# Kernel optimization log

Hardware: AMD Instinct MI355X
Metric: run time of the kernel (lower is better)

## Reference

```python
import jax, jax.numpy as jnp
import numpy as np

NEG_INF = -9e15  # matches torch's -9000000000000000.0 mask value
ALPHA = 0.2      # LeakyReLU negative slope


def setup_inputs() -> dict:
    key = jax.random.key(0)
    k1, k2, k3, k4 = jax.random.split(key, 4)
    B, N, Fin, Fout = 8, 2048, 256, 256
    h = jax.random.normal(k1, (B, N, Fin), dtype=jnp.float32)
    adj = jax.random.randint(k2, (B, N, N), 0, 2, dtype=jnp.int32)
    # xavier_uniform with gain=1.414
    limW = 1.414 * np.sqrt(6.0 / (Fin + Fout))
    W = jax.random.uniform(k3, (Fin, Fout), minval=-limW, maxval=limW, dtype=jnp.float32)
    lima = 1.414 * np.sqrt(6.0 / (2 * Fout + 1))
    a = jax.random.uniform(k4, (2 * Fout, 1), minval=-lima, maxval=lima, dtype=jnp.float32)
    return {"h": h, "adj": adj, "W": W, "a": a}


def reference(h, adj, W, a):
    # h: (B, N, Fin), adj: (B, N, N), W: (Fin, Fout), a: (2*Fout, 1)
    Fout = W.shape[1]
    Wh = jnp.einsum('bni,io->bno', h, W)                 # (B, N, Fout)
    # e[b,i,j] = leakyrelu(Wh[b,i] @ a1 + Wh[b,j] @ a2) -- equivalent to the
    # original concat([Wh_i, Wh_j]) @ a without the O(N^2 * 2F) intermediate.
    e1 = Wh @ a[:Fout, 0]                                # (B, N)
    e2 = Wh @ a[Fout:, 0]                                # (B, N)
    e = jax.nn.leaky_relu(e1[:, :, None] + e2[:, None, :], negative_slope=ALPHA)
    masked = jnp.where(adj > 0, e, NEG_INF)
    attention = jax.nn.softmax(masked, axis=-1)          # (B, N, N)
    # dropout omitted (deterministic eval-mode reference)
    h_prime = jnp.einsum('bij,bjo->bio', attention, Wh)  # (B, N, Fout)
    return jax.nn.elu(h_prime), attention
```

## Files before the change

kernel.cpp:

```cpp
#include <hip/hip_runtime.h>
#include <hip/hip_bf16.h>
#include <stdint.h>

#define NEG_INF -9.0e15f
#define LRELU_ALPHA 0.2f
#define LOG2E 1.442695040888963f

using bf16x8  = __attribute__((ext_vector_type(8))) short;
using f32x4   = __attribute__((ext_vector_type(4))) float;
using short4v = __attribute__((ext_vector_type(4))) short;
using int4v   = __attribute__((ext_vector_type(4))) int;
using float4v = __attribute__((ext_vector_type(4))) float;
using uint2v  = __attribute__((ext_vector_type(2))) unsigned;
using uint4v  = __attribute__((ext_vector_type(4))) unsigned;

static __device__ __forceinline__ short f2bf(float f) {
  unsigned u = __builtin_bit_cast(unsigned, f);
  u = u + 0x7FFFu + ((u >> 16) & 1u);
  return (short)(u >> 16);
}
static __device__ __forceinline__ unsigned cvtpk_bf16(float lo, float hi) {
  unsigned r;
  asm volatile("v_cvt_pk_bf16_f32 %0, %1, %2" : "=v"(r) : "v"(lo), "v"(hi));
  return r;
}
static __device__ __forceinline__ void gload16(const void* g, void* l) {
  __builtin_amdgcn_global_load_lds((const __attribute__((address_space(1))) void*)g,
                                   (__attribute__((address_space(3))) void*)l, 16, 0, 0);
}

__global__ __launch_bounds__(256) void prep_kernel(
    const float* __restrict__ W, const float* __restrict__ a,
    short* __restrict__ W_t, float* __restrict__ aW1, float* __restrict__ aW2)
{
  const int bid = blockIdx.x;
  const int tid = threadIdx.x;
  if (bid < 16) {
    __shared__ float t[64][65];
    const int m0 = (bid & 3) * 64, n0 = (bid >> 2) * 64;
    const int rr = tid >> 3, cc = (tid & 7) * 8;
#pragma unroll
    for (int p = 0; p < 2; ++p) {
      int row = rr + p * 32;
      const float* sp = W + (m0 + row) * 256 + n0 + cc;
      float4v v0 = *(const float4v*)sp;
      float4v v1 = *(const float4v*)(sp + 4);
#pragma unroll
      for (int j = 0; j < 4; ++j) { t[row][cc + j] = v0[j]; t[row][cc + 4 + j] = v1[j]; }
    }
    __syncthreads();
#pragma unroll
    for (int p = 0; p < 2; ++p) {
      int orow = rr + p * 32;
      short vv[8] __attribute__((aligned(16)));
#pragma unroll
      for (int j = 0; j < 8; ++j) vv[j] = f2bf(t[cc + j][orow]);
      short* dp = W_t + (n0 + orow) * 256 + m0 + cc;
      *(int4v*)dp = *(const int4v*)vv;
    }
  } else {
    const int r8 = tid >> 3, o4 = (tid & 7) * 4;
    float s1[8] = {}, s2[8] = {};
#pragma unroll
    for (int rp = 0; rp < 8; ++rp) {
      int row = r8 + rp * 32;
#pragma unroll
      for (int k = 0; k < 8; ++k) {
        int o = o4 + k * 32;
        float4v wv = *(const float4v*)(W + row * 256 + o);
        float4v a1 = *(const float4v*)(a + o);
        float4v a2 = *(const float4v*)(a + 256 + o);
#pragma unroll
        for (int e = 0; e < 4; ++e) { s1[rp] += wv[e] * a1[e]; s2[rp] += wv[e] * a2[e]; }
      }
    }
#pragma unroll
    for (int rp = 0; rp < 8; ++rp) {
#pragma unroll
      for (int off = 4; off > 0; off >>= 1) {
        s1[rp] += __shfl_xor(s1[rp], off, 64);
        s2[rp] += __shfl_xor(s2[rp], off, 64);
      }
      if ((tid & 7) == 0) { aW1[r8 + rp * 32] = s1[rp]; aW2[r8 + rp * 32] = s2[rp]; }
    }
  }
}

__global__ __launch_bounds__(256) void evec2_kernel(
    const float* __restrict__ h, const float* __restrict__ aW1,
    const float* __restrict__ aW2, float* __restrict__ e1, float* __restrict__ e2)
{
  const int wid = threadIdx.x >> 6, lane = threadIdx.x & 63;
  const long long r = (long long)blockIdx.x * 4 + wid;
  float4v hv  = *(const float4v*)(h + r * 256 + lane * 4);
  float4v a1v = *(const float4v*)(aW1 + lane * 4);
  float4v a2v = *(const float4v*)(aW2 + lane * 4);
  float s1 = 0.f, s2 = 0.f;
#pragma unroll
  for (int k = 0; k < 4; ++k) { s1 += hv[k] * a1v[k]; s2 += hv[k] * a2v[k]; }
#pragma unroll
  for (int off = 32; off > 0; off >>= 1) {
    s1 += __shfl_xor(s1, off, 64);
    s2 += __shfl_xor(s2, off, 64);
  }
  if (lane == 0) { e1[r] = s1; e2[r] = s2; }
}

__global__ __launch_bounds__(256) void gemm_h_kernel(
    const float* __restrict__ A, const short* __restrict__ Bt,
    short* __restrict__ Wht)
{
  __shared__ short As[128 * 32];
  __shared__ short Bs[128 * 32];
  __shared__ short T[128][136];
  const int m0 = blockIdx.x * 128, n0 = blockIdx.y * 128;
  const int tid = threadIdx.x;
  const int w = tid >> 6, lane = tid & 63;
  const int wr = w >> 1, wc = w & 1;
  const int g = lane >> 4, lr = lane & 15;

  f32x4 acc[4][4] = {};

  for (int k0 = 0; k0 < 256; k0 += 32) {
    __syncthreads();
#pragma unroll
    for (int q = 0; q < 2; ++q) {
      int c = q * 256 + tid;
      int row = c >> 2, kq = (c & 3) << 3;
      const float* ap = A + (long long)(m0 + row) * 256 + k0 + kq;
      float4v u0 = *(const float4v*)ap;
      float4v u1 = *(const float4v*)(ap + 4);
      uint4v uv;
      uv[0] = cvtpk_bf16(u0[0], u0[1]);
      uv[1] = cvtpk_bf16(u0[2], u0[3]);
      uv[2] = cvtpk_bf16(u1[0], u1[1]);
      uv[3] = cvtpk_bf16(u1[2], u1[3]);
      *(bf16x8*)(As + c * 8) = __builtin_bit_cast(bf16x8, uv);
    }
#pragma unroll
    for (int q = 0; q < 2; ++q) {
      int p = w * 2 + q;
      int c = p * 64 + lane;
      int row = c >> 2, kq = (c & 3) << 3;
      gload16(Bt + (long long)(n0 + row) * 256 + k0 + kq, Bs + p * 512);
    }
    __syncthreads();

    bf16x8 af[4], bfr[4];
#pragma unroll
    for (int i = 0; i < 4; ++i) {
      af[i]  = *(const bf16x8*)(As + (wr * 64 + i * 16 + lr) * 32 + 8 * g);
      bfr[i] = *(const bf16x8*)(Bs + (wc * 64 + i * 16 + lr) * 32 + 8 * g);
    }
#pragma unroll
    for (int i = 0; i < 4; ++i)
#pragma unroll
      for (int j = 0; j < 4; ++j)
        acc[i][j] = __builtin_amdgcn_mfma_f32_16x16x32_bf16(af[i], bfr[j], acc[i][j], 0, 0, 0);
  }

  __syncthreads();
#pragma unroll
  for (int i = 0; i < 4; ++i) {
    int row_base = wr * 64 + i * 16 + 4 * g;
#pragma unroll
    for (int j = 0; j < 4; ++j) {
      int col = wc * 64 + j * 16 + lr;
#pragma unroll
      for (int r = 0; r < 4; ++r)
        T[col][row_base + r] = f2bf(acc[i][j][r]);
    }
  }
  __syncthreads();
  const int b = m0 >> 11, mloc = m0 & 2047;
  short* wb = Wht + (long long)b * 524288 + mloc;
#pragma unroll
  for (int p = 0; p < 8; ++p) {
    int c = (tid >> 4) + p * 16;
    int off = (tid & 15) * 8;
    bf16x8 v = *(const bf16x8*)(&T[c][off]);
    *(bf16x8*)(wb + (long long)(n0 + c) * 2048 + off) = v;
  }
}

__global__ __launch_bounds__(256) void pack_stats_kernel(
    const int* __restrict__ adj, const float* __restrict__ e1,
    const float* __restrict__ e2, unsigned char* __restrict__ mask,
    float* __restrict__ Lr, float* __restrict__ Dr)
{
  const int i = blockIdx.x;
  const int b = blockIdx.y;
  const long long row = (long long)b * 2048 + i;
  const int tid = threadIdx.x;
  const int wid = tid >> 6, lane = tid & 63;
  const int j0 = tid * 8;

  const int*   arow = adj + row * 2048 + j0;
  const float  ei   = e1[row];
  const float* e2b  = e2 + b * 2048 + j0;

  int4v   a0 = *(const int4v*)(arow);
  int4v   a1 = *(const int4v*)(arow + 4);
  float4v f0 = *(const float4v*)(e2b);
  float4v f1 = *(const float4v*)(e2b + 4);

  float s[8]; unsigned byte = 0u;
#pragma unroll
  for (int k = 0; k < 8; ++k) {
    float x = ei + (k < 4 ? f0[k] : f1[k - 4]);
    float v = fmaxf(x, LRELU_ALPHA * x);
    int  ad = (k < 4 ? a0[k] : a1[k - 4]);
    if (ad > 0) { s[k] = v; byte |= (1u << k); } else s[k] = NEG_INF;
  }
  float m = s[0];
#pragma unroll
  for (int k = 1; k < 8; ++k) m = fmaxf(m, s[k]);
#pragma unroll
  for (int off = 32; off > 0; off >>= 1) m = fmaxf(m, __shfl_xor(m, off, 64));

  __shared__ float wmax[4], wsum[4];
  if (lane == 0) wmax[wid] = m;
  __syncthreads();
  const float M = fmaxf(fmaxf(wmax[0], wmax[1]), fmaxf(wmax[2], wmax[3]));
  const bool empty = (M == NEG_INF);

  mask[row * 256 + tid] = empty ? (unsigned char)0xFF : (unsigned char)byte;

  float t = 0.f;
#pragma unroll
  for (int k = 0; k < 8; ++k) t += __expf(s[k] - M);
#pragma unroll
  for (int off = 32; off > 0; off >>= 1) t += __shfl_xor(t, off, 64);
  if (lane == 0) wsum[wid] = t;
  __syncthreads();
  if (tid == 0) {
    const float S = wsum[0] + wsum[1] + wsum[2] + wsum[3];
    Lr[row] = empty ? 0.0f : LOG2E;
    Dr[row] = empty ? -11.0f : (-M * LOG2E - __log2f(S));
  }
}

__global__ __launch_bounds__(256, 4) void pv_kernel(
    const unsigned char* __restrict__ mask, const float* __restrict__ e1,
    const float* __restrict__ e2, const float* __restrict__ Lr,
    const float* __restrict__ Dr, const short* __restrict__ Bt,
    float* __restrict__ attnw, float* __restrict__ C)
{
  __shared__ short As0[32 * 32],  As1[32 * 32];
  __shared__ short Bs0[256 * 32], Bs1[256 * 32];
  const int bid = blockIdx.x;
  const int bz  = bid & 7;
  const int M0  = (bid >> 3) << 5;
  const int tid = threadIdx.x;
  const int w = tid >> 6, lane = tid & 63;
  const int g = lane >> 4, lr = lane & 15;

  const long long rb = (long long)bz * 2048;
  Bt    += (long long)bz * 524288;
  attnw += (long long)bz * 4194304;
  C     += (long long)bz * 524288;

  const int pr = tid >> 3, k4 = (tid & 7) << 2;
  const int prow = M0 + pr;
  const float E1p = e1[rb + prow];
  const float Lp  = Lr[rb + prow];
  const float Dp  = Dr[rb + prow];
  const unsigned char* mrow = mask + (rb + prow) * 256;
  float* arow = attnw + (long long)prow * 2048;
  const int kc = k4 >> 3;
  const int as_off = pr * 32 + ((kc ^ ((pr >> 1) & 3)) << 3) + (k4 & 7);
  const float* e2b = e2 + rb;

  const int bcol_off = lane >> 2;
  const int bchunk   = (lane & 3) ^ ((lane >> 3) & 3);

  f32x4 acc[2][4] = {};

  auto STAGE = [&](short* BsD, short* AsD, int k0) {
#pragma unroll
    for (int q = 0; q < 4; ++q) {
      int pp = w * 4 + q;
      int col = pp * 16 + bcol_off;
      gload16(Bt + (long long)col * 2048 + k0 + bchunk * 8, BsD + pp * 512);
    }
    const unsigned by = (unsigned)(mrow[(k0 + k4) >> 3] >> (k4 & 7)) & 0xFu;
    const int kk = k0 + k4;
    float4v ev = *(const float4v*)(e2b + kk);
    float p4[4];
#pragma unroll
    for (int e = 0; e < 4; ++e) {
      float x = E1p + ev[e];
      float v = fmaxf(x, LRELU_ALPHA * x);
      float P = __builtin_amdgcn_exp2f(fmaf(v, Lp, Dp));
      p4[e] = ((by >> e) & 1u) ? P : 0.0f;
    }
    float4v o;
#pragma unroll
    for (int e = 0; e < 4; ++e) o[e] = p4[e];
    *(float4v*)(arow + kk) = o;
    uint2v uv;
    uv[0] = cvtpk_bf16(p4[0], p4[1]);
    uv[1] = cvtpk_bf16(p4[2], p4[3]);
    *(uint2v*)(AsD + as_off) = uv;
  };

  auto COMPUTE = [&](const short* BsD, const short* AsD) {
    bf16x8 af[2], bfr[4];
#pragma unroll
    for (int i = 0; i < 2; ++i) {
      int row = i * 16 + lr;
      af[i] = *(const bf16x8*)(AsD + row * 32 + ((g ^ ((row >> 1) & 3)) << 3));
    }
#pragma unroll
    for (int j = 0; j < 4; ++j) {
      int col = w * 64 + j * 16 + lr;
      bfr[j] = *(const bf16x8*)(BsD + col * 32 + ((g ^ ((col >> 1) & 3)) << 3));
    }
#pragma unroll
    for (int i = 0; i < 2; ++i)
#pragma unroll
      for (int j = 0; j < 4; ++j)
        acc[i][j] = __builtin_amdgcn_mfma_f32_16x16x32_bf16(af[i], bfr[j], acc[i][j], 0, 0, 0);
  };

  STAGE(Bs0, As0, 0);
  __syncthreads();
  for (int t = 0; t < 64; t += 2) {
    STAGE(Bs1, As1, (t + 1) * 32);
    COMPUTE(Bs0, As0);
    __syncthreads();
    if (t + 2 < 64) STAGE(Bs0, As0, (t + 2) * 32);
    COMPUTE(Bs1, As1);
    __syncthreads();
  }

#pragma unroll
  for (int i = 0; i < 2; ++i) {
    int row_base = M0 + i * 16 + 4 * g;
#pragma unroll
    for (int j = 0; j < 4; ++j) {
      int col = w * 64 + j * 16 + lr;
#pragma unroll
      for (int r = 0; r < 4; ++r) {
        float v = acc[i][j][r];
        v = (v > 0.f) ? v : (__expf(v) - 1.f);
        C[(long long)(row_base + r) * 256 + col] = v;
      }
    }
  }
}

extern "C" void kernel_launch(void* const* d_in, const int* in_sizes, int n_in,
                              void* d_out, int out_size, void* d_ws, size_t ws_size,
                              hipStream_t stream)
{
  const float* h   = (const float*)d_in[0];
  const int*   adj = (const int*)d_in[1];
  const float* W   = (const float*)d_in[2];
  const float* a   = (const float*)d_in[3];

  float* hp_out   = (float*)d_out;
  float* attn_out = hp_out + 4194304LL;

  unsigned char* mask = (unsigned char*)d_ws;
  short* W_t  = (short*)(mask + 4194304);
  short* Wh_t = W_t + 65536;
  float* e1   = (float*)(Wh_t + 4194304);
  float* e2   = e1 + 16384;
  float* Lr   = e2 + 16384;
  float* Dr   = Lr + 16384;
  float* aW1  = Dr + 16384;
  float* aW2  = aW1 + 256;

  prep_kernel<<<17, 256, 0, stream>>>(W, a, W_t, aW1, aW2);
  evec2_kernel<<<4096, 256, 0, stream>>>(h, aW1, aW2, e1, e2);
  gemm_h_kernel<<<dim3(128, 2), 256, 0, stream>>>(h, W_t, Wh_t);
  pack_stats_kernel<<<dim3(2048, 8), 256, 0, stream>>>(adj, e1, e2, mask, Lr, Dr);
  pv_kernel<<<512, 256, 0, stream>>>(mask, e1, e2, Lr, Dr, Wh_t, attn_out, hp_out);
}
```

Baseline: 123.0 us.

## Fuse e-vector dot products into Wh GEMM and stage e2/mask in LDS

Result: faster. 109.3 us (-11.2%).

```diff
diff --git a/kernel.cpp b/kernel.cpp
--- a/kernel.cpp
+++ b/kernel.cpp
@@ -86,29 +86,10 @@
   }
 }
 
-__global__ __launch_bounds__(256) void evec2_kernel(
-    const float* __restrict__ h, const float* __restrict__ aW1,
-    const float* __restrict__ aW2, float* __restrict__ e1, float* __restrict__ e2)
-{
-  const int wid = threadIdx.x >> 6, lane = threadIdx.x & 63;
-  const long long r = (long long)blockIdx.x * 4 + wid;
-  float4v hv  = *(const float4v*)(h + r * 256 + lane * 4);
-  float4v a1v = *(const float4v*)(aW1 + lane * 4);
-  float4v a2v = *(const float4v*)(aW2 + lane * 4);
-  float s1 = 0.f, s2 = 0.f;
-#pragma unroll
-  for (int k = 0; k < 4; ++k) { s1 += hv[k] * a1v[k]; s2 += hv[k] * a2v[k]; }
-#pragma unroll
-  for (int off = 32; off > 0; off >>= 1) {
-    s1 += __shfl_xor(s1, off, 64);
-    s2 += __shfl_xor(s2, off, 64);
-  }
-  if (lane == 0) { e1[r] = s1; e2[r] = s2; }
-}
-
 __global__ __launch_bounds__(256) void gemm_h_kernel(
     const float* __restrict__ A, const short* __restrict__ Bt,
-    short* __restrict__ Wht)
+    short* __restrict__ Wht, const float* __restrict__ aW1,
+    const float* __restrict__ aW2, float* __restrict__ e1, float* __restrict__ e2)
 {
   __shared__ short As[128 * 32];
   __shared__ short Bs[128 * 32];
@@ -118,8 +99,10 @@
   const int w = tid >> 6, lane = tid & 63;
   const int wr = w >> 1, wc = w & 1;
   const int g = lane >> 4, lr = lane & 15;
+  const bool doE = (blockIdx.y == 0);
 
   f32x4 acc[4][4] = {};
+  float s1q[2] = {0.f, 0.f}, s2q[2] = {0.f, 0.f};
 
   for (int k0 = 0; k0 < 256; k0 += 32) {
     __syncthreads();
@@ -130,6 +113,17 @@
       const float* ap = A + (long long)(m0 + row) * 256 + k0 + kq;
       float4v u0 = *(const float4v*)ap;
       float4v u1 = *(const float4v*)(ap + 4);
+      if (doE) {
+        float4v w1a = *(const float4v*)(aW1 + k0 + kq);
+        float4v w1b = *(const float4v*)(aW1 + k0 + kq + 4);
+        float4v w2a = *(const float4v*)(aW2 + k0 + kq);
+        float4v w2b = *(const float4v*)(aW2 + k0 + kq + 4);
+#pragma unroll
+        for (int e = 0; e < 4; ++e) {
+          s1q[q] += u0[e] * w1a[e] + u1[e] * w1b[e];
+          s2q[q] += u0[e] * w2a[e] + u1[e] * w2b[e];
+        }
+      }
       uint4v uv;
       uv[0] = cvtpk_bf16(u0[0], u0[1]);
       uv[1] = cvtpk_bf16(u0[2], u0[3]);
@@ -159,6 +153,19 @@
         acc[i][j] = __builtin_amdgcn_mfma_f32_16x16x32_bf16(af[i], bfr[j], acc[i][j], 0, 0, 0);
   }
 
+  if (doE) {
+#pragma unroll
+    for (int q = 0; q < 2; ++q) {
+      float a1 = s1q[q], a2 = s2q[q];
+      a1 += __shfl_xor(a1, 1, 64); a1 += __shfl_xor(a1, 2, 64);
+      a2 += __shfl_xor(a2, 1, 64); a2 += __shfl_xor(a2, 2, 64);
+      if ((tid & 3) == 0) {
+        int row = m0 + q * 64 + (tid >> 2);
+        e1[row] = a1; e2[row] = a2;
+      }
+    }
+  }
+
   __syncthreads();
 #pragma unroll
   for (int i = 0; i < 4; ++i) {
@@ -240,7 +247,7 @@
   }
 }
 
-__global__ __launch_bounds__(256, 4) void pv_kernel(
+__global__ __launch_bounds__(256, 3) void pv_kernel(
     const unsigned char* __restrict__ mask, const float* __restrict__ e1,
     const float* __restrict__ e2, const float* __restrict__ Lr,
     const float* __restrict__ Dr, const short* __restrict__ Bt,
@@ -248,6 +255,8 @@
 {
   __shared__ short As0[32 * 32],  As1[32 * 32];
   __shared__ short Bs0[256 * 32], Bs1[256 * 32];
+  __shared__ float e2s[2048];
+  __shared__ unsigned char msk[32 * 256];
   const int bid = blockIdx.x;
   const int bz  = bid & 7;
   const int M0  = (bid >> 3) << 5;
@@ -265,14 +274,23 @@
   const float E1p = e1[rb + prow];
   const float Lp  = Lr[rb + prow];
   const float Dp  = Dr[rb + prow];
-  const unsigned char* mrow = mask + (rb + prow) * 256;
   float* arow = attnw + (long long)prow * 2048;
   const int kc = k4 >> 3;
   const int as_off = pr * 32 + ((kc ^ ((pr >> 1) & 3)) << 3) + (k4 & 7);
-  const float* e2b = e2 + rb;
 
   const int bcol_off = lane >> 2;
   const int bchunk   = (lane & 3) ^ ((lane >> 3) & 3);
+
+  {
+    const float* e2g = e2 + rb;
+    const unsigned char* mg = mask + (rb + M0) * 256;
+#pragma unroll
+    for (int q = 0; q < 2; ++q) {
+      int p = w * 2 + q;
+      gload16(e2g + p * 256 + lane * 4, (char*)e2s + p * 1024);
+      gload16(mg  + p * 1024 + lane * 16, (char*)msk + p * 1024);
+    }
+  }
 
   f32x4 acc[2][4] = {};
 
@@ -283,9 +301,9 @@
       int col = pp * 16 + bcol_off;
       gload16(Bt + (long long)col * 2048 + k0 + bchunk * 8, BsD + pp * 512);
     }
-    const unsigned by = (unsigned)(mrow[(k0 + k4) >> 3] >> (k4 & 7)) & 0xFu;
     const int kk = k0 + k4;
-    float4v ev = *(const float4v*)(e2b + kk);
+    const unsigned by = (unsigned)(msk[pr * 256 + (kk >> 3)] >> (k4 & 7)) & 0xFu;
+    float4v ev = *(const float4v*)(e2s + kk);
     float p4[4];
 #pragma unroll
     for (int e = 0; e < 4; ++e) {
@@ -323,6 +341,7 @@
         acc[i][j] = __builtin_amdgcn_mfma_f32_16x16x32_bf16(af[i], bfr[j], acc[i][j], 0, 0, 0);
   };
 
+  __syncthreads();
   STAGE(Bs0, As0, 0);
   __syncthreads();
   for (int t = 0; t < 64; t += 2) {
@@ -373,8 +392,7 @@
   float* aW2  = aW1 + 256;
 
   prep_kernel<<<17, 256, 0, stream>>>(W, a, W_t, aW1, aW2);
-  evec2_kernel<<<4096, 256, 0, stream>>>(h, aW1, aW2, e1, e2);
-  gemm_h_kernel<<<dim3(128, 2), 256, 0, stream>>>(h, W_t, Wh_t);
+  gemm_h_kernel<<<dim3(128, 2), 256, 0, stream>>>(h, W_t, Wh_t, aW1, aW2, e1, e2);
   pack_stats_kernel<<<dim3(2048, 8), 256, 0, stream>>>(adj, e1, e2, mask, Lr, Dr);
   pv_kernel<<<512, 256, 0, stream>>>(mask, e1, e2, Lr, Dr, Wh_t, attn_out, hp_out);
 }
```

## Merge Wh GEMM with mask/stats kernel; stage e2 and mask in LDS for PV

Applied to the files above, without the earlier changes.

Measured after the change: 111.0 us. -9.7%, faster.

```diff
diff --git a/kernel.cpp b/kernel.cpp
--- a/kernel.cpp
+++ b/kernel.cpp
@@ -106,141 +106,141 @@
   if (lane == 0) { e1[r] = s1; e2[r] = s2; }
 }
 
-__global__ __launch_bounds__(256) void gemm_h_kernel(
+__global__ __launch_bounds__(256) void merged_kernel(
     const float* __restrict__ A, const short* __restrict__ Bt,
-    short* __restrict__ Wht)
-{
-  __shared__ short As[128 * 32];
-  __shared__ short Bs[128 * 32];
-  __shared__ short T[128][136];
-  const int m0 = blockIdx.x * 128, n0 = blockIdx.y * 128;
+    short* __restrict__ Wht, const int* __restrict__ adj,
+    const float* __restrict__ e1, const float* __restrict__ e2,
+    unsigned char* __restrict__ mask, float* __restrict__ Lr, float* __restrict__ Dr)
+{
+  __shared__ short POOL[128 * 136];
+  __shared__ float wmax[4], wsum[4];
+  const int bid = blockIdx.x;
   const int tid = threadIdx.x;
-  const int w = tid >> 6, lane = tid & 63;
-  const int wr = w >> 1, wc = w & 1;
-  const int g = lane >> 4, lr = lane & 15;
-
-  f32x4 acc[4][4] = {};
-
-  for (int k0 = 0; k0 < 256; k0 += 32) {
-    __syncthreads();
-#pragma unroll
-    for (int q = 0; q < 2; ++q) {
-      int c = q * 256 + tid;
-      int row = c >> 2, kq = (c & 3) << 3;
-      const float* ap = A + (long long)(m0 + row) * 256 + k0 + kq;
-      float4v u0 = *(const float4v*)ap;
-      float4v u1 = *(const float4v*)(ap + 4);
-      uint4v uv;
-      uv[0] = cvtpk_bf16(u0[0], u0[1]);
-      uv[1] = cvtpk_bf16(u0[2], u0[3]);
-      uv[2] = cvtpk_bf16(u1[0], u1[1]);
-      uv[3] = cvtpk_bf16(u1[2], u1[3]);
-      *(bf16x8*)(As + c * 8) = __builtin_bit_cast(bf16x8, uv);
-    }
-#pragma unroll
-    for (int q = 0; q < 2; ++q) {
-      int p = w * 2 + q;
-      int c = p * 64 + lane;
-      int row = c >> 2, kq = (c & 3) << 3;
-      gload16(Bt + (long long)(n0 + row) * 256 + k0 + kq, Bs + p * 512);
-    }
-    __syncthreads();
-
-    bf16x8 af[4], bfr[4];
+
+  if (bid < 256) {
+    short* As = POOL;
+    short* Bs = POOL + 4096;
+    const int m0 = (bid & 127) * 128, n0 = (bid >> 7) * 128;
+    const int w = tid >> 6, lane = tid & 63;
+    const int wr = w >> 1, wc = w & 1;
+    const int g = lane >> 4, lr = lane & 15;
+
+    f32x4 acc[4][4] = {};
+
+    for (int k0 = 0; k0 < 256; k0 += 32) {
+      __syncthreads();
+#pragma unroll
+      for (int q = 0; q < 2; ++q) {
+        int c = q * 256 + tid;
+        int row = c >> 2, kq = (c & 3) << 3;
+        const float* ap = A + (long long)(m0 + row) * 256 + k0 + kq;
+        float4v u0 = *(const float4v*)ap;
+        float4v u1 = *(const float4v*)(ap + 4);
+        uint4v uv;
+        uv[0] = cvtpk_bf16(u0[0], u0[1]);
+        uv[1] = cvtpk_bf16(u0[2], u0[3]);
+        uv[2] = cvtpk_bf16(u1[0], u1[1]);
+        uv[3] = cvtpk_bf16(u1[2], u1[3]);
+        *(bf16x8*)(As + c * 8) = __builtin_bit_cast(bf16x8, uv);
+      }
+#pragma unroll
+      for (int q = 0; q < 2; ++q) {
+        int p = w * 2 + q;
+        int c = p * 64 + lane;
+        int row = c >> 2, kq = (c & 3) << 3;
+        gload16(Bt + (long long)(n0 + row) * 256 + k0 + kq, Bs + p * 512);
+      }
+      __syncthreads();
+
+      bf16x8 af[4], bfr[4];
+#pragma unroll
+      for (int i = 0; i < 4; ++i) {
+        af[i]  = *(const bf16x8*)(As + (wr * 64 + i * 16 + lr) * 32 + 8 * g);
+        bfr[i] = *(const bf16x8*)(Bs + (wc * 64 + i * 16 + lr) * 32 + 8 * g);
+      }
+#pragma unroll
+      for (int i = 0; i < 4; ++i)
+#pragma unroll
+        for (int j = 0; j < 4; ++j)
+          acc[i][j] = __builtin_amdgcn_mfma_f32_16x16x32_bf16(af[i], bfr[j], acc[i][j], 0, 0, 0);
+    }
+
+    __syncthreads();
 #pragma unroll
     for (int i = 0; i < 4; ++i) {
-      af[i]  = *(const bf16x8*)(As + (wr * 64 + i * 16 + lr) * 32 + 8 * g);
-      bfr[i] = *(const bf16x8*)(Bs + (wc * 64 + i * 16 + lr) * 32 + 8 * g);
-    }
-#pragma unroll
-    for (int i = 0; i < 4; ++i)
-#pragma unroll
-      for (int j = 0; j < 4; ++j)
-        acc[i][j] = __builtin_amdgcn_mfma_f32_16x16x32_bf16(af[i], bfr[j], acc[i][j], 0, 0, 0);
-  }
-
-  __syncthreads();
-#pragma unroll
-  for (int i = 0; i < 4; ++i) {
-    int row_base = wr * 64 + i * 16 + 4 * g;
-#pragma unroll
-    for (int j = 0; j < 4; ++j) {
-      int col = wc * 64 + j * 16 + lr;
-#pragma unroll
-      for (int r = 0; r < 4; ++r)
-        T[col][row_base + r] = f2bf(acc[i][j][r]);
-    }
-  }
-  __syncthreads();
-  const int b = m0 >> 11, mloc = m0 & 2047;
-  short* wb = Wht + (long long)b * 524288 + mloc;
-#pragma unroll
-  for (int p = 0; p < 8; ++p) {
-    int c = (tid >> 4) + p * 16;
-    int off = (tid & 15) * 8;
-    bf16x8 v = *(const bf16x8*)(&T[c][off]);
-    *(bf16x8*)(wb + (long long)(n0 + c) * 2048 + off) = v;
-  }
-}
-
-__global__ __launch_bounds__(256) void pack_stats_kernel(
-    const int* __restrict__ adj, const float* __restrict__ e1,
-    const float* __restrict__ e2, unsigned char* __restrict__ mask,
-    float* __restrict__ Lr, float* __restrict__ Dr)
-{
-  const int i = blockIdx.x;
-  const int b = blockIdx.y;
-  const long long row = (long long)b * 2048 + i;
-  const int tid = threadIdx.x;
-  const int wid = tid >> 6, lane = tid & 63;
-  const int j0 = tid * 8;
-
-  const int*   arow = adj + row * 2048 + j0;
-  const float  ei   = e1[row];
-  const float* e2b  = e2 + b * 2048 + j0;
-
-  int4v   a0 = *(const int4v*)(arow);
-  int4v   a1 = *(const int4v*)(arow + 4);
-  float4v f0 = *(const float4v*)(e2b);
-  float4v f1 = *(const float4v*)(e2b + 4);
-
-  float s[8]; unsigned byte = 0u;
-#pragma unroll
-  for (int k = 0; k < 8; ++k) {
-    float x = ei + (k < 4 ? f0[k] : f1[k - 4]);
-    float v = fmaxf(x, LRELU_ALPHA * x);
-    int  ad = (k < 4 ? a0[k] : a1[k - 4]);
-    if (ad > 0) { s[k] = v; byte |= (1u << k); } else s[k] = NEG_INF;
-  }
-  float m = s[0];
-#pragma unroll
-  for (int k = 1; k < 8; ++k) m = fmaxf(m, s[k]);
-#pragma unroll
-  for (int off = 32; off > 0; off >>= 1) m = fmaxf(m, __shfl_xor(m, off, 64));
-
-  __shared__ float wmax[4], wsum[4];
-  if (lane == 0) wmax[wid] = m;
-  __syncthreads();
-  const float M = fmaxf(fmaxf(wmax[0], wmax[1]), fmaxf(wmax[2], wmax[3]));
-  const bool empty = (M == NEG_INF);
-
-  mask[row * 256 + tid] = empty ? (unsigned char)0xFF : (unsigned char)byte;
-
-  float t = 0.f;
-#pragma unroll
-  for (int k = 0; k < 8; ++k) t += __expf(s[k] - M);
-#pragma unroll
-  for (int off = 32; off > 0; off >>= 1) t += __shfl_xor(t, off, 64);
-  if (lane == 0) wsum[wid] = t;
-  __syncthreads();
-  if (tid == 0) {
-    const float S = wsum[0] + wsum[1] + wsum[2] + wsum[3];
-    Lr[row] = empty ? 0.0f : LOG2E;
-    Dr[row] = empty ? -11.0f : (-M * LOG2E - __log2f(S));
-  }
-}
-
-__global__ __launch_bounds__(256, 4) void pv_kernel(
+      int row_base = wr * 64 + i * 16 + 4 * g;
+#pragma unroll
+      for (int j = 0; j < 4; ++j) {
+        int col = wc * 64 + j * 16 + lr;
+#pragma unroll
+        for (int r = 0; r < 4; ++r)
+          POOL[col * 136 + row_base + r] = f2bf(acc[i][j][r]);
+      }
+    }
+    __syncthreads();
+    const int b = m0 >> 11, mloc = m0 & 2047;
+    short* wb = Wht + (long long)b * 524288 + mloc;
+#pragma unroll
+    for (int p = 0; p < 8; ++p) {
+      int c = (tid >> 4) + p * 16;
+      int off = (tid & 15) * 8;
+      bf16x8 v = *(const bf16x8*)(&POOL[c * 136 + off]);
+      *(bf16x8*)(wb + (long long)(n0 + c) * 2048 + off) = v;
+    }
+  } else {
+    const int idx = bid - 256;
+    const int i = idx & 2047;
+    const int b = idx >> 11;
+    const long long row = (long long)b * 2048 + i;
+    const int wid = tid >> 6, lane = tid & 63;
+    const int j0 = tid * 8;
+
+    const int*   arow = adj + row * 2048 + j0;
+    const float  ei   = e1[row];
+    const float* e2b  = e2 + b * 2048 + j0;
+
+    int4v   a0 = *(const int4v*)(arow);
+    int4v   a1 = *(const int4v*)(arow + 4);
+    float4v f0 = *(const float4v*)(e2b);
+    float4v f1 = *(const float4v*)(e2b + 4);
+
+    float s[8]; unsigned byte = 0u;
+#pragma unroll
+    for (int k = 0; k < 8; ++k) {
+      float x = ei + (k < 4 ? f0[k] : f1[k - 4]);
+      float v = fmaxf(x, LRELU_ALPHA * x);
+      int  ad = (k < 4 ? a0[k] : a1[k - 4]);
+      if (ad > 0) { s[k] = v; byte |= (1u << k); } else s[k] = NEG_INF;
+    }
+    float m = s[0];
+#pragma unroll
+    for (int k = 1; k < 8; ++k) m = fmaxf(m, s[k]);
+#pragma unroll
+    for (int off = 32; off > 0; off >>= 1) m = fmaxf(m, __shfl_xor(m, off, 64));
+
+    if (lane == 0) wmax[wid] = m;
+    __syncthreads();
+    const float M = fmaxf(fmaxf(wmax[0], wmax[1]), fmaxf(wmax[2], wmax[3]));
+    const bool empty = (M == NEG_INF);
+
+    mask[row * 256 + tid] = empty ? (unsigned char)0xFF : (unsigned char)byte;
+
+    float t = 0.f;
+#pragma unroll
+    for (int k = 0; k < 8; ++k) t += __expf(s[k] - M);
+#pragma unroll
+    for (int off = 32; off > 0; off >>= 1) t += __shfl_xor(t, off, 64);
+    if (lane == 0) wsum[wid] = t;
+    __syncthreads();
+    if (tid == 0) {
+      const float S = wsum[0] + wsum[1] + wsum[2] + wsum[3];
+      Lr[row] = empty ? 0.0f : LOG2E;
+      Dr[row] = empty ? -11.0f : (-M * LOG2E - __log2f(S));
+    }
+  }
+}
+
+__global__ __launch_bounds__(256, 3) void pv_kernel(
     const unsigned char* __restrict__ mask, const float* __restrict__ e1,
     const float* __restrict__ e2, const float* __restrict__ Lr,
     const float* __restrict__ Dr, const short* __restrict__ Bt,
@@ -248,6 +248,8 @@
 {
   __shared__ short As0[32 * 32],  As1[32 * 32];
   __shared__ short Bs0[256 * 32], Bs1[256 * 32];
+  __shared__ float e2s[2048];
+  __shared__ unsigned char msk[32 * 256];
   const int bid = blockIdx.x;
   const int bz  = bid & 7;
   const int M0  = (bid >> 3) << 5;
@@ -265,14 +267,23 @@
   const float E1p = e1[rb + prow];
   const float Lp  = Lr[rb + prow];
   const float Dp  = Dr[rb + prow];
-  const unsigned char* mrow = mask + (rb + prow) * 256;
   float* arow = attnw + (long long)prow * 2048;
   const int kc = k4 >> 3;
   const int as_off = pr * 32 + ((kc ^ ((pr >> 1) & 3)) << 3) + (k4 & 7);
-  const float* e2b = e2 + rb;
 
   const int bcol_off = lane >> 2;
   const int bchunk   = (lane & 3) ^ ((lane >> 3) & 3);
+
+  {
+    const float* e2g = e2 + rb;
+    const unsigned char* mg = mask + (rb + M0) * 256;
+#pragma unroll
+    for (int q = 0; q < 2; ++q) {
+      int p = w * 2 + q;
+      gload16(e2g + p * 256 + lane * 4, (char*)e2s + p * 1024);
+      gload16(mg  + p * 1024 + lane * 16, (char*)msk + p * 1024);
+    }
+  }
 
   f32x4 acc[2][4] = {};
 
@@ -283,9 +294,9 @@
       int col = pp * 16 + bcol_off;
       gload16(Bt + (long long)col * 2048 + k0 + bchunk * 8, BsD + pp * 512);
     }
-    const unsigned by = (unsigned)(mrow[(k0 + k4) >> 3] >> (k4 & 7)) & 0xFu;
     const int kk = k0 + k4;
-    float4v ev = *(const float4v*)(e2b + kk);
+    const unsigned by = (unsigned)(msk[pr * 256 + (kk >> 3)] >> (k4 & 7)) & 0xFu;
+    float4v ev = *(const float4v*)(e2s + kk);
     float p4[4];
 #pragma unroll
     for (int e = 0; e < 4; ++e) {
@@ -323,6 +334,7 @@
         acc[i][j] = __builtin_amdgcn_mfma_f32_16x16x32_bf16(af[i], bfr[j], acc[i][j], 0, 0, 0);
   };
 
+  __syncthreads();
   STAGE(Bs0, As0, 0);
   __syncthreads();
   for (int t = 0; t < 64; t += 2) {
@@ -374,7 +386,6 @@
 
   prep_kernel<<<17, 256, 0, stream>>>(W, a, W_t, aW1, aW2);
   evec2_kernel<<<4096, 256, 0, stream>>>(h, aW1, aW2, e1, e2);
-  gemm_h_kernel<<<dim3(128, 2), 256, 0, stream>>>(h, W_t, Wh_t);
-  pack_stats_kernel<<<dim3(2048, 8), 256, 0, stream>>>(adj, e1, e2, mask, Lr, Dr);
+  merged_kernel<<<16640, 256, 0, stream>>>(h, W_t, Wh_t, adj, e1, e2, mask, Lr, Dr);
   pv_kernel<<<512, 256, 0, stream>>>(mask, e1, e2, Lr, Dr, Wh_t, attn_out, hp_out);
 }
```
